# Kernel tuning notes

Measured on AMD Instinct MI355X. Metric: run time of the kernel, lower is better.

Reference implementation:

```python
import jax, jax.numpy as jnp
import numpy as np

N, G, E, D, H = 50000, 1000, 400000, 128, 256


def _sample_negatives(edge_index, batch, rng):
    # Vectorized equivalent of the torch per-edge loop: for each positive edge,
    # draw a dst in the same graph as src, excluding src itself and src's
    # existing neighbors, via 8 rounds of rejection sampling.
    src = edge_index[0]
    counts = np.bincount(batch, minlength=G)
    starts = np.concatenate([[0], np.cumsum(counts)[:-1]])
    g = batch[src]
    edge_keys = np.unique(edge_index[0].astype(np.int64) * N + edge_index[1])
    dst = src.copy()
    valid = np.zeros(E, dtype=bool)
    for _ in range(8):
        cand = starts[g] + rng.integers(0, counts[g])
        ok = (cand != src) & ~np.isin(src.astype(np.int64) * N + cand, edge_keys)
        take = ok & ~valid
        dst = np.where(take, cand, dst)
        valid |= ok
    fallback = starts[g] + (src - starts[g] + 1) % counts[g]  # deterministic in-graph node != src (when graph>1)
    dst = np.where(valid, dst, fallback)
    return np.stack([src, dst]).astype(np.int64)


def setup_inputs() -> dict:
    rng = np.random.default_rng(0)
    batch = np.sort(rng.integers(0, G, size=N)).astype(np.int64)  # contiguous graph ids
    counts = np.bincount(batch, minlength=G)
    starts = np.concatenate([[0], np.cumsum(counts)[:-1]])
    src = rng.integers(0, N, size=E)
    gsrc = batch[src]
    dst = starts[gsrc] + rng.integers(0, counts[gsrc])  # same-graph positive edges
    edge_index = np.stack([src, dst]).astype(np.int64)
    neg_edge_index = _sample_negatives(edge_index, batch, rng)

    key = jax.random.key(0)
    ks = jax.random.split(key, 4)
    x = jax.random.normal(ks[0], (N, D), jnp.float32)
    w1 = jax.random.normal(ks[1], (2 * D, H), jnp.float32) / np.sqrt(2 * D)
    w2 = jax.random.normal(ks[2], (H, H // 2), jnp.float32) / np.sqrt(H)
    w3 = jax.random.normal(ks[3], (H // 2, 1), jnp.float32) / np.sqrt(H // 2)
    return {
        "x": x,
        "edge_index": jnp.asarray(edge_index),
        "batch": jnp.asarray(batch),
        "neg_edge_index": jnp.asarray(neg_edge_index),
        "w1": w1, "b1": jnp.zeros((H,), jnp.float32),
        "g1": jnp.ones((H,), jnp.float32), "be1": jnp.zeros((H,), jnp.float32),
        "w2": w2, "b2": jnp.zeros((H // 2,), jnp.float32),
        "g2": jnp.ones((H // 2,), jnp.float32), "be2": jnp.zeros((H // 2,), jnp.float32),
        "w3": w3, "b3": jnp.zeros((1,), jnp.float32),
    }


def _layernorm(h, g, b, eps=1e-5):
    m = jnp.mean(h, axis=-1, keepdims=True)
    v = jnp.mean(jnp.square(h - m), axis=-1, keepdims=True)
    return (h - m) * jax.lax.rsqrt(v + eps) * g + b


def _edge_mlp(feat, w1, b1, g1, be1, w2, b2, g2, be2, w3, b3):
    h = jax.nn.relu(_layernorm(feat @ w1 + b1, g1, be1))
    h = jax.nn.relu(_layernorm(h @ w2 + b2, g2, be2))
    return jax.nn.sigmoid(h @ w3 + b3)


def reference(x, edge_index, batch, neg_edge_index, w1, b1, g1, be1, w2, b2, g2, be2, w3, b3):
    # batch is consumed by the (setup-time) negative sampler; kept for signature fidelity.
    all_idx = jnp.concatenate([edge_index, neg_edge_index], axis=1)  # [2, 2E]
    feat = jnp.concatenate([x[all_idx[0]], x[all_idx[1]]], axis=-1)  # [2E, 2D]
    pred = _edge_mlp(feat, w1, b1, g1, be1, w2, b2, g2, be2, w3, b3)  # [2E, 1]
    num_pos = edge_index.shape[1]
    num_neg = neg_edge_index.shape[1]
    labels = jnp.concatenate(
        [jnp.ones((num_pos, 1), pred.dtype), jnp.zeros((num_neg, 1), pred.dtype)], axis=0
    )
    return pred, labels
```

## Files before the change

### kernel.cpp

```cpp
#include <hip/hip_runtime.h>
#include <math.h>
#include <stdint.h>

#define NN    50000
#define EPOS  400000
#define ROWS  800000
#define DIM   128
#define D2    256
#define H1C   256
#define H2C   128
#define MT    64
#define NTH   512

typedef __bf16 bf16;
typedef __bf16 bf16x8 __attribute__((ext_vector_type(8)));
typedef __bf16 bf16x4 __attribute__((ext_vector_type(4)));
typedef float  f32x4  __attribute__((ext_vector_type(4)));

#define XB_N   (NN*DIM)
#define W1F_E  XB_N
#define W1F_N  (H1C*D2)
#define W2F_E  (XB_N + W1F_N)
#define W2F_N  (H2C*H1C)
#define WS_NEEDED ((size_t)(XB_N + W1F_N + W2F_N) * 2)

#define AOFF  0
#define SCR   32768
#define SCR2  34816
#define CFOFF 35840
#define SMEM_BYTES 40960

__device__ __forceinline__ void gll16(const void* g, void* l) {
    __builtin_amdgcn_global_load_lds(
        (const __attribute__((address_space(1))) void*)g,
        (__attribute__((address_space(3))) void*)l, 16, 0, 0);
}

__global__ void preconv(const float* __restrict__ x, const float* __restrict__ w1,
                        const float* __restrict__ w2, bf16* __restrict__ ws) {
    int i = blockIdx.x * 256 + threadIdx.x;
    if (i < XB_N) { ws[i] = (bf16)x[i]; return; }
    i -= XB_N;
    if (i < W1F_N) {
        int j = i & 7, l = (i >> 3) & 63, ct = i >> 9;
        int c = ct >> 4, t = ct & 15;
        int n = t * 16 + (l & 15);
        int k = c * 32 + (l >> 4) * 8 + j;
        ws[W1F_E + i] = (bf16)w1[k * H1C + n];
        return;
    }
    i -= W1F_N;
    if (i < W2F_N) {
        int j = i & 7, l = (i >> 3) & 63, ct = i >> 9;
        int c = ct >> 3, t = ct & 7;
        int n = t * 16 + (l & 15);
        int k = c * 32 + (l >> 4) * 8 + j;
        ws[W2F_E + i] = (bf16)w2[k * H2C + n];
    }
}

__global__ __launch_bounds__(NTH, 4) void lp_mfma8(
    const bf16* __restrict__ xb, const bf16* __restrict__ w1f, const bf16* __restrict__ w2f,
    const int*  __restrict__ ei, const int* __restrict__ nei,
    const float* __restrict__ b1, const float* __restrict__ g1, const float* __restrict__ be1,
    const float* __restrict__ b2, const float* __restrict__ g2, const float* __restrict__ be2,
    const float* __restrict__ w3, const float* __restrict__ b3,
    float* __restrict__ out)
{
    extern __shared__ char smem[];
    const int tid  = threadIdx.x;
    const int lane = tid & 63;
    const int w    = tid >> 6;
    const int wm   = w >> 2;
    const int wn   = w & 3;
    const int gr0  = blockIdx.x * MT;
    const int l15  = lane & 15;
    const int l4   = lane >> 4;

    #pragma unroll
    for (int ii = 0; ii < 4; ++ii) {
        const int i = w * 4 + ii;
        uint32_t doff = (uint32_t)(i << 10) + (uint32_t)(lane << 4);
        uint32_t loff = doff ^ (((doff >> 9) & 7u) << 4);
        int row = loff >> 9;
        int inb = loff & 511;
        int gr  = gr0 + row;
        int node;
        if (inb < 256) { node = (gr < EPOS) ? ei[gr]        : nei[gr - EPOS]; }
        else           { node = (gr < EPOS) ? ei[EPOS + gr] : nei[gr]; inb -= 256; }
        gll16((const char*)xb + (((size_t)node) << 8) + inb, smem + AOFF + (i << 10));
    }

    for (int i = tid; i < 1280; i += NTH) {
        float v;
        if      (i < 256)  v = b1[i];
        else if (i < 512)  v = g1[i - 256];
        else if (i < 768)  v = be1[i - 512];
        else if (i < 896)  v = b2[i - 768];
        else if (i < 1024) v = g2[i - 896];
        else if (i < 1152) v = be2[i - 1024];
        else               v = w3[i - 1152];
        *(float*)(smem + CFOFF + i * 4) = v;
    }

    uint32_t abase[2], asw[2];
    #pragma unroll
    for (int mi = 0; mi < 2; ++mi) {
        int row = (wm << 5) + (mi << 4) + l15;
        abase[mi] = (uint32_t)row << 9;
        asw[mi]   = (uint32_t)(row & 7) << 4;
    }
    const uint32_t koff  = (uint32_t)l4 << 4;
    const uint32_t c1off = ((uint32_t)wn << 8) + ((uint32_t)l4 << 4);
    const uint32_t c2off = ((uint32_t)wn << 7) + ((uint32_t)l4 << 4);

    __syncthreads();

    f32x4 acc1s[2][4] = {};
    const bf16* bp1 = w1f + (wn << 11) + (lane << 3);
    #pragma unroll
    for (int c = 0; c < 8; ++c) {
        bf16x8 af[2];
        #pragma unroll
        for (int mi = 0; mi < 2; ++mi)
            af[mi] = *(const bf16x8*)(smem + AOFF + ((abase[mi] + ((uint32_t)c << 6) + koff) ^ asw[mi]));
        #pragma unroll
        for (int ni = 0; ni < 4; ++ni) {
            bf16x8 bfr = *(const bf16x8*)(bp1 + (c << 13) + (ni << 9));
            #pragma unroll
            for (int mi = 0; mi < 2; ++mi)
                acc1s[mi][ni] = __builtin_amdgcn_mfma_f32_16x16x32_bf16(
                    bfr, af[mi], acc1s[mi][ni], 0, 0, 0);
        }
    }

    #pragma unroll
    for (int mi = 0; mi < 2; ++mi) {
        float s1 = 0.f, s2 = 0.f;
        #pragma unroll
        for (int ni = 0; ni < 4; ++ni) {
            f32x4 bias = *(const f32x4*)(smem + CFOFF + c1off + (ni << 6));
            #pragma unroll
            for (int j = 0; j < 4; ++j) {
                float v = acc1s[mi][ni][j] + bias[j];
                acc1s[mi][ni][j] = v;
                s1 += v; s2 += v * v;
            }
        }
        s1 += __shfl_xor(s1, 16); s1 += __shfl_xor(s1, 32);
        s2 += __shfl_xor(s2, 16); s2 += __shfl_xor(s2, 32);
        if (l4 == 0) {
            int row = (wm << 5) + (mi << 4) + l15;
            *(float2*)(smem + SCR + (row << 5) + (wn << 3)) = make_float2(s1, s2);
        }
    }
    __syncthreads();

    #pragma unroll
    for (int mi = 0; mi < 2; ++mi) {
        int row = (wm << 5) + (mi << 4) + l15;
        f32x4 p0 = *(const f32x4*)(smem + SCR + (row << 5));
        f32x4 p1 = *(const f32x4*)(smem + SCR + (row << 5) + 16);
        float s1 = p0[0] + p0[2] + p1[0] + p1[2];
        float s2 = p0[1] + p0[3] + p1[1] + p1[3];
        float mean = s1 * (1.f / 256.f);
        float var  = s2 * (1.f / 256.f) - mean * mean;
        float rstd = rsqrtf(var + 1e-5f);
        #pragma unroll
        for (int ni = 0; ni < 4; ++ni) {
            f32x4 gv  = *(const f32x4*)(smem + CFOFF + 1024 + c1off + (ni << 6));
            f32x4 bev = *(const f32x4*)(smem + CFOFF + 2048 + c1off + (ni << 6));
            bf16x4 hb;
            #pragma unroll
            for (int j = 0; j < 4; ++j) {
                float h = (acc1s[mi][ni][j] - mean) * rstd * gv[j] + bev[j];
                hb[j] = (bf16)fmaxf(h, 0.f);
            }
            uint32_t byte = ((uint32_t)row << 9) + ((uint32_t)wn << 7) + ((uint32_t)ni << 5) + ((uint32_t)l4 << 3);
            byte ^= ((byte >> 9) & 7u) << 4;
            *(bf16x4*)(smem + AOFF + byte) = hb;
        }
    }
    __syncthreads();

    f32x4 acc2s[2][2] = {};
    const bf16* bp2 = w2f + (wn << 10) + (lane << 3);
    #pragma unroll
    for (int c = 0; c < 8; ++c) {
        bf16x8 a2[2];
        #pragma unroll
        for (int mi = 0; mi < 2; ++mi)
            a2[mi] = *(const bf16x8*)(smem + AOFF + ((abase[mi] + ((uint32_t)c << 6) + koff) ^ asw[mi]));
        #pragma unroll
        for (int ni = 0; ni < 2; ++ni) {
            bf16x8 b2r = *(const bf16x8*)(bp2 + (c << 12) + (ni << 9));
            #pragma unroll
            for (int mi = 0; mi < 2; ++mi)
                acc2s[mi][ni] = __builtin_amdgcn_mfma_f32_16x16x32_bf16(
                    b2r, a2[mi], acc2s[mi][ni], 0, 0, 0);
        }
    }

    #pragma unroll
    for (int mi = 0; mi < 2; ++mi) {
        float s1 = 0.f, s2 = 0.f;
        #pragma unroll
        for (int ni = 0; ni < 2; ++ni) {
            f32x4 bias = *(const f32x4*)(smem + CFOFF + 3072 + c2off + (ni << 6));
            #pragma unroll
            for (int j = 0; j < 4; ++j) {
                float v = acc2s[mi][ni][j] + bias[j];
                acc2s[mi][ni][j] = v;
                s1 += v; s2 += v * v;
            }
        }
        s1 += __shfl_xor(s1, 16); s1 += __shfl_xor(s1, 32);
        s2 += __shfl_xor(s2, 16); s2 += __shfl_xor(s2, 32);
        if (l4 == 0) {
            int row = (wm << 5) + (mi << 4) + l15;
            *(float2*)(smem + SCR + (row << 5) + (wn << 3)) = make_float2(s1, s2);
        }
    }
    __syncthreads();

    #pragma unroll
    for (int mi = 0; mi < 2; ++mi) {
        int row = (wm << 5) + (mi << 4) + l15;
        f32x4 p0 = *(const f32x4*)(smem + SCR + (row << 5));
        f32x4 p1 = *(const f32x4*)(smem + SCR + (row << 5) + 16);
        float s1 = p0[0] + p0[2] + p1[0] + p1[2];
        float s2 = p0[1] + p0[3] + p1[1] + p1[3];
        float mean = s1 * (1.f / 128.f);
        float var  = s2 * (1.f / 128.f) - mean * mean;
        float rstd = rsqrtf(var + 1e-5f);
        float zp = 0.f;
        #pragma unroll
        for (int ni = 0; ni < 2; ++ni) {
            f32x4 gv  = *(const f32x4*)(smem + CFOFF + 3584 + c2off + (ni << 6));
            f32x4 bev = *(const f32x4*)(smem + CFOFF + 4096 + c2off + (ni << 6));
            f32x4 wv  = *(const f32x4*)(smem + CFOFF + 4608 + c2off + (ni << 6));
            #pragma unroll
            for (int j = 0; j < 4; ++j) {
                float h = (acc2s[mi][ni][j] - mean) * rstd * gv[j] + bev[j];
                h = fmaxf(h, 0.f);
                zp += h * wv[j];
            }
        }
        zp += __shfl_xor(zp, 16); zp += __shfl_xor(zp, 32);
        if (l4 == 0)
            *(float*)(smem + SCR2 + (row << 4) + (wn << 2)) = zp;
    }
    __syncthreads();

    if (wn == 0) {
        const float b3s = b3[0];
        #pragma unroll
        for (int mi = 0; mi < 2; ++mi) {
            int row = (wm << 5) + (mi << 4) + l15;
            int gr  = gr0 + row;
            if (l4 == 0) {
                f32x4 zv = *(const f32x4*)(smem + SCR2 + (row << 4));
                float z = zv[0] + zv[1] + zv[2] + zv[3] + b3s;
                out[gr] = 1.f / (1.f + expf(-z));
            } else if (l4 == 1) {
                out[ROWS + gr] = (gr < EPOS) ? 1.f : 0.f;
            }
        }
    }
}

#define TILE  32
#define PAD   264
__global__ __launch_bounds__(256, 4) void lp_fused(
    const float* __restrict__ x, const int* __restrict__ ei, const int* __restrict__ nei,
    const float* __restrict__ w1, const float* __restrict__ b1,
    const float* __restrict__ g1, const float* __restrict__ be1,
    const float* __restrict__ w2, const float* __restrict__ b2,
    const float* __restrict__ g2, const float* __restrict__ be2,
    const float* __restrict__ w3, const float* __restrict__ b3,
    float* __restrict__ out)
{
    __shared__ float lds[TILE][PAD];
    const int t = threadIdx.x, e = t >> 3, jg = t & 7;
    const int row = blockIdx.x * TILE + e;
    {
        int src, dst;
        if (row < EPOS) { src = ei[row];         dst = ei[EPOS + row]; }
        else            { src = nei[row - EPOS]; dst = nei[row]; }
        const float* base = (jg < 4) ? (x + src * DIM + jg * 32) : (x + dst * DIM + (jg - 4) * 32);
        const float4* b4 = (const float4*)base;
        #pragma unroll
        for (int s = 0; s < 8; ++s) *(float4*)&lds[e][jg * 32 + s * 4] = b4[s];
    }
    __syncthreads();
    float acc[32];
    #pragma unroll
    for (int i = 0; i < 32; ++i) acc[i] = 0.f;
    const int j0 = jg * 32;
    for (int k4 = 0; k4 < D2 / 4; ++k4) {
        float4 a4 = *(const float4*)&lds[e][k4 * 4];
        float av[4] = {a4.x, a4.y, a4.z, a4.w};
        #pragma unroll
        for (int kk = 0; kk < 4; ++kk) {
            const float a = av[kk];
            const float4* wr = (const float4*)(w1 + (k4 * 4 + kk) * H1C + j0);
            #pragma unroll
            for (int ii = 0; ii < 8; ++ii) {
                float4 wv = wr[ii];
                acc[ii*4+0] += a*wv.x; acc[ii*4+1] += a*wv.y; acc[ii*4+2] += a*wv.z; acc[ii*4+3] += a*wv.w;
            }
        }
    }
    float s1 = 0.f, s2 = 0.f;
    #pragma unroll
    for (int i = 0; i < 32; ++i) { float h = acc[i] + b1[j0+i]; acc[i] = h; s1 += h; s2 += h*h; }
    #pragma unroll
    for (int m = 1; m < 8; m <<= 1) { s1 += __shfl_xor(s1, m, 8); s2 += __shfl_xor(s2, m, 8); }
    float mean = s1 * (1.f/256.f), var = s2 * (1.f/256.f) - mean*mean, rstd = rsqrtf(var + 1e-5f);
    __syncthreads();
    #pragma unroll
    for (int i = 0; i < 32; ++i)
        lds[e][j0+i] = fmaxf((acc[i]-mean)*rstd*g1[j0+i]+be1[j0+i], 0.f);
    __syncthreads();
    float acc2[16];
    #pragma unroll
    for (int i = 0; i < 16; ++i) acc2[i] = 0.f;
    const int q0 = jg * 16;
    for (int k4 = 0; k4 < H1C / 4; ++k4) {
        float4 a4 = *(const float4*)&lds[e][k4 * 4];
        float av[4] = {a4.x, a4.y, a4.z, a4.w};
        #pragma unroll
        for (int kk = 0; kk < 4; ++kk) {
            const float a = av[kk];
            const float4* wr = (const float4*)(w2 + (k4 * 4 + kk) * H2C + q0);
            #pragma unroll
            for (int ii = 0; ii < 4; ++ii) {
                float4 wv = wr[ii];
                acc2[ii*4+0] += a*wv.x; acc2[ii*4+1] += a*wv.y; acc2[ii*4+2] += a*wv.z; acc2[ii*4+3] += a*wv.w;
            }
        }
    }
    s1 = 0.f; s2 = 0.f;
    #pragma unroll
    for (int i = 0; i < 16; ++i) { float h = acc2[i] + b2[q0+i]; acc2[i] = h; s1 += h; s2 += h*h; }
    #pragma unroll
    for (int m = 1; m < 8; m <<= 1) { s1 += __shfl_xor(s1, m, 8); s2 += __shfl_xor(s2, m, 8); }
    mean = s1 * (1.f/128.f); var = s2 * (1.f/128.f) - mean*mean; rstd = rsqrtf(var + 1e-5f);
    float zp = 0.f;
    #pragma unroll
    for (int i = 0; i < 16; ++i) {
        float h = fmaxf((acc2[i]-mean)*rstd*g2[q0+i]+be2[q0+i], 0.f);
        zp += h * w3[q0+i];
    }
    #pragma unroll
    for (int m = 1; m < 8; m <<= 1) zp += __shfl_xor(zp, m, 8);
    if (jg == 0) out[row] = 1.f / (1.f + expf(-(zp + b3[0])));
    if (jg == 1) out[ROWS + row] = (row < EPOS) ? 1.f : 0.f;
}

extern "C" void kernel_launch(void* const* d_in, const int* in_sizes, int n_in,
                              void* d_out, int out_size, void* d_ws, size_t ws_size,
                              hipStream_t stream) {
    const float* x   = (const float*)d_in[0];
    const int*   ei  = (const int*)d_in[1];
    const int*   nei = (const int*)d_in[3];
    const float* w1  = (const float*)d_in[4];
    const float* b1  = (const float*)d_in[5];
    const float* g1  = (const float*)d_in[6];
    const float* be1 = (const float*)d_in[7];
    const float* w2  = (const float*)d_in[8];
    const float* b2  = (const float*)d_in[9];
    const float* g2  = (const float*)d_in[10];
    const float* be2 = (const float*)d_in[11];
    const float* w3  = (const float*)d_in[12];
    const float* b3  = (const float*)d_in[13];
    float* out = (float*)d_out;

    if (ws_size >= WS_NEEDED) {
        bf16* ws = (bf16*)d_ws;
        const int total = XB_N + W1F_N + W2F_N;
        hipLaunchKernelGGL(preconv, dim3((total + 255) / 256), dim3(256), 0, stream,
                           x, w1, w2, ws);
        hipFuncSetAttribute((const void*)lp_mfma8,
                            hipFuncAttributeMaxDynamicSharedMemorySize, SMEM_BYTES);
        hipLaunchKernelGGL(lp_mfma8, dim3(ROWS / MT), dim3(NTH), SMEM_BYTES, stream,
                           ws, ws + W1F_E, ws + W2F_E, ei, nei,
                           b1, g1, be1, b2, g2, be2, w3, b3, out);
    } else {
        hipLaunchKernelGGL(lp_fused, dim3(ROWS / TILE), dim3(256), 0, stream,
                           x, ei, nei, w1, b1, g1, be1, w2, b2, g2, be2, w3, b3, out);
    }
}
```

Before: 264.9 us.

## Make MLP kernel persistent with double-buffered gather prefetch of next tile

Launches a fixed grid of 512 blocks, each looping over row tiles in a grid-stride loop. It uses two LDS buffers so the global_load_lds gather of the next tile's node features overlaps compute on the current tile. Bias is now folded into the MFMA accumulator initialisation instead of being added after the matmul. LDS per block roughly doubles, which lowers resident blocks per CU, and 25-vs-24 tiles per block adds some tail imbalance.

After: 872.6 us. 229% more time.

```diff
diff --git a/kernel.cpp b/kernel.cpp
--- a/kernel.cpp
+++ b/kernel.cpp
@@ -11,6 +11,8 @@
 #define H2C   128
 #define MT    64
 #define NTH   512
+#define TILES (ROWS/MT)
+#define GRID  512
 
 typedef __bf16 bf16;
 typedef __bf16 bf16x8 __attribute__((ext_vector_type(8)));
@@ -24,11 +26,10 @@
 #define W2F_N  (H2C*H1C)
 #define WS_NEEDED ((size_t)(XB_N + W1F_N + W2F_N) * 2)
 
-#define AOFF  0
-#define SCR   32768
-#define SCR2  34816
-#define CFOFF 35840
-#define SMEM_BYTES 40960
+#define SCR   65536
+#define SCR2  67584
+#define CFOFF 68608
+#define SMEM_BYTES 73728
 
 __device__ __forceinline__ void gll16(const void* g, void* l) {
     __builtin_amdgcn_global_load_lds(
@@ -59,7 +60,7 @@
     }
 }
 
-__global__ __launch_bounds__(NTH, 4) void lp_mfma8(
+__global__ __launch_bounds__(NTH, 4) void lp_mfma10(
     const bf16* __restrict__ xb, const bf16* __restrict__ w1f, const bf16* __restrict__ w2f,
     const int*  __restrict__ ei, const int* __restrict__ nei,
     const float* __restrict__ b1, const float* __restrict__ g1, const float* __restrict__ be1,
@@ -73,23 +74,24 @@
     const int w    = tid >> 6;
     const int wm   = w >> 2;
     const int wn   = w & 3;
-    const int gr0  = blockIdx.x * MT;
     const int l15  = lane & 15;
     const int l4   = lane >> 4;
 
-    #pragma unroll
-    for (int ii = 0; ii < 4; ++ii) {
-        const int i = w * 4 + ii;
-        uint32_t doff = (uint32_t)(i << 10) + (uint32_t)(lane << 4);
-        uint32_t loff = doff ^ (((doff >> 9) & 7u) << 4);
-        int row = loff >> 9;
-        int inb = loff & 511;
-        int gr  = gr0 + row;
-        int node;
-        if (inb < 256) { node = (gr < EPOS) ? ei[gr]        : nei[gr - EPOS]; }
-        else           { node = (gr < EPOS) ? ei[EPOS + gr] : nei[gr]; inb -= 256; }
-        gll16((const char*)xb + (((size_t)node) << 8) + inb, smem + AOFF + (i << 10));
-    }
+    auto stage = [&](int tile, uint32_t base) {
+        #pragma unroll
+        for (int ii = 0; ii < 4; ++ii) {
+            const int i = w * 4 + ii;
+            uint32_t doff = (uint32_t)(i << 10) + (uint32_t)(lane << 4);
+            uint32_t loff = doff ^ (((doff >> 9) & 7u) << 4);
+            int row = loff >> 9;
+            int inb = loff & 511;
+            int gr  = tile * MT + row;
+            int node;
+            if (inb < 256) { node = (gr < EPOS) ? ei[gr]        : nei[gr - EPOS]; }
+            else           { node = (gr < EPOS) ? ei[EPOS + gr] : nei[gr]; inb -= 256; }
+            gll16((const char*)xb + (((size_t)node) << 8) + inb, smem + base + (i << 10));
+        }
+    };
 
     for (int i = tid; i < 1280; i += NTH) {
         float v;
@@ -102,6 +104,7 @@
         else               v = w3[i - 1152];
         *(float*)(smem + CFOFF + i * 4) = v;
     }
+    stage(blockIdx.x, 0);
 
     uint32_t abase[2], asw[2];
     #pragma unroll
@@ -113,159 +116,171 @@
     const uint32_t koff  = (uint32_t)l4 << 4;
     const uint32_t c1off = ((uint32_t)wn << 8) + ((uint32_t)l4 << 4);
     const uint32_t c2off = ((uint32_t)wn << 7) + ((uint32_t)l4 << 4);
+    const float b3s = b3[0];
 
     __syncthreads();
 
-    f32x4 acc1s[2][4] = {};
-    const bf16* bp1 = w1f + (wn << 11) + (lane << 3);
-    #pragma unroll
-    for (int c = 0; c < 8; ++c) {
-        bf16x8 af[2];
-        #pragma unroll
-        for (int mi = 0; mi < 2; ++mi)
-            af[mi] = *(const bf16x8*)(smem + AOFF + ((abase[mi] + ((uint32_t)c << 6) + koff) ^ asw[mi]));
-        #pragma unroll
-        for (int ni = 0; ni < 4; ++ni) {
-            bf16x8 bfr = *(const bf16x8*)(bp1 + (c << 13) + (ni << 9));
-            #pragma unroll
-            for (int mi = 0; mi < 2; ++mi)
-                acc1s[mi][ni] = __builtin_amdgcn_mfma_f32_16x16x32_bf16(
-                    bfr, af[mi], acc1s[mi][ni], 0, 0, 0);
-        }
-    }
-
-    #pragma unroll
-    for (int mi = 0; mi < 2; ++mi) {
-        float s1 = 0.f, s2 = 0.f;
+    int cur = 0;
+    for (int t = blockIdx.x; t < TILES; t += GRID) {
+        const uint32_t abuf = (uint32_t)cur << 15;
+        const int nt = t + GRID;
+        if (nt < TILES) stage(nt, abuf ^ 32768u);
+
+        f32x4 acc1s[2][4];
         #pragma unroll
         for (int ni = 0; ni < 4; ++ni) {
             f32x4 bias = *(const f32x4*)(smem + CFOFF + c1off + (ni << 6));
-            #pragma unroll
-            for (int j = 0; j < 4; ++j) {
-                float v = acc1s[mi][ni][j] + bias[j];
-                acc1s[mi][ni][j] = v;
-                s1 += v; s2 += v * v;
-            }
-        }
-        s1 += __shfl_xor(s1, 16); s1 += __shfl_xor(s1, 32);
-        s2 += __shfl_xor(s2, 16); s2 += __shfl_xor(s2, 32);
-        if (l4 == 0) {
+            acc1s[0][ni] = bias; acc1s[1][ni] = bias;
+        }
+        const bf16* bp1 = w1f + (wn << 11) + (lane << 3);
+        #pragma unroll
+        for (int c = 0; c < 8; ++c) {
+            bf16x8 af[2];
+            #pragma unroll
+            for (int mi = 0; mi < 2; ++mi)
+                af[mi] = *(const bf16x8*)(smem + abuf + ((abase[mi] + ((uint32_t)c << 6) + koff) ^ asw[mi]));
+            #pragma unroll
+            for (int ni = 0; ni < 4; ++ni) {
+                bf16x8 bfr = *(const bf16x8*)(bp1 + (c << 13) + (ni << 9));
+                #pragma unroll
+                for (int mi = 0; mi < 2; ++mi)
+                    acc1s[mi][ni] = __builtin_amdgcn_mfma_f32_16x16x32_bf16(
+                        bfr, af[mi], acc1s[mi][ni], 0, 0, 0);
+            }
+        }
+
+        #pragma unroll
+        for (int mi = 0; mi < 2; ++mi) {
+            float s1 = 0.f, s2 = 0.f;
+            #pragma unroll
+            for (int ni = 0; ni < 4; ++ni)
+                #pragma unroll
+                for (int j = 0; j < 4; ++j) {
+                    float v = acc1s[mi][ni][j];
+                    s1 += v; s2 += v * v;
+                }
+            s1 += __shfl_xor(s1, 16); s1 += __shfl_xor(s1, 32);
+            s2 += __shfl_xor(s2, 16); s2 += __shfl_xor(s2, 32);
+            if (l4 == 0) {
+                int row = (wm << 5) + (mi << 4) + l15;
+                *(float2*)(smem + SCR + (row << 5) + (wn << 3)) = make_float2(s1, s2);
+            }
+        }
+        __syncthreads();
+
+        #pragma unroll
+        for (int mi = 0; mi < 2; ++mi) {
             int row = (wm << 5) + (mi << 4) + l15;
-            *(float2*)(smem + SCR + (row << 5) + (wn << 3)) = make_float2(s1, s2);
-        }
-    }
-    __syncthreads();
-
-    #pragma unroll
-    for (int mi = 0; mi < 2; ++mi) {
-        int row = (wm << 5) + (mi << 4) + l15;
-        f32x4 p0 = *(const f32x4*)(smem + SCR + (row << 5));
-        f32x4 p1 = *(const f32x4*)(smem + SCR + (row << 5) + 16);
-        float s1 = p0[0] + p0[2] + p1[0] + p1[2];
-        float s2 = p0[1] + p0[3] + p1[1] + p1[3];
-        float mean = s1 * (1.f / 256.f);
-        float var  = s2 * (1.f / 256.f) - mean * mean;
-        float rstd = rsqrtf(var + 1e-5f);
-        #pragma unroll
-        for (int ni = 0; ni < 4; ++ni) {
-            f32x4 gv  = *(const f32x4*)(smem + CFOFF + 1024 + c1off + (ni << 6));
-            f32x4 bev = *(const f32x4*)(smem + CFOFF + 2048 + c1off + (ni << 6));
-            bf16x4 hb;
-            #pragma unroll
-            for (int j = 0; j < 4; ++j) {
-                float h = (acc1s[mi][ni][j] - mean) * rstd * gv[j] + bev[j];
-                hb[j] = (bf16)fmaxf(h, 0.f);
-            }
-            uint32_t byte = ((uint32_t)row << 9) + ((uint32_t)wn << 7) + ((uint32_t)ni << 5) + ((uint32_t)l4 << 3);
-            byte ^= ((byte >> 9) & 7u) << 4;
-            *(bf16x4*)(smem + AOFF + byte) = hb;
-        }
-    }
-    __syncthreads();
-
-    f32x4 acc2s[2][2] = {};
-    const bf16* bp2 = w2f + (wn << 10) + (lane << 3);
-    #pragma unroll
-    for (int c = 0; c < 8; ++c) {
-        bf16x8 a2[2];
-        #pragma unroll
-        for (int mi = 0; mi < 2; ++mi)
-            a2[mi] = *(const bf16x8*)(smem + AOFF + ((abase[mi] + ((uint32_t)c << 6) + koff) ^ asw[mi]));
-        #pragma unroll
-        for (int ni = 0; ni < 2; ++ni) {
-            bf16x8 b2r = *(const bf16x8*)(bp2 + (c << 12) + (ni << 9));
-            #pragma unroll
-            for (int mi = 0; mi < 2; ++mi)
-                acc2s[mi][ni] = __builtin_amdgcn_mfma_f32_16x16x32_bf16(
-                    b2r, a2[mi], acc2s[mi][ni], 0, 0, 0);
-        }
-    }
-
-    #pragma unroll
-    for (int mi = 0; mi < 2; ++mi) {
-        float s1 = 0.f, s2 = 0.f;
+            f32x4 p0 = *(const f32x4*)(smem + SCR + (row << 5));
+            f32x4 p1 = *(const f32x4*)(smem + SCR + (row << 5) + 16);
+            float s1 = p0[0] + p0[2] + p1[0] + p1[2];
+            float s2 = p0[1] + p0[3] + p1[1] + p1[3];
+            float mean = s1 * (1.f / 256.f);
+            float var  = s2 * (1.f / 256.f) - mean * mean;
+            float rstd = rsqrtf(var + 1e-5f);
+            #pragma unroll
+            for (int ni = 0; ni < 4; ++ni) {
+                f32x4 gv  = *(const f32x4*)(smem + CFOFF + 1024 + c1off + (ni << 6));
+                f32x4 bev = *(const f32x4*)(smem + CFOFF + 2048 + c1off + (ni << 6));
+                bf16x4 hb;
+                #pragma unroll
+                for (int j = 0; j < 4; ++j) {
+                    float h = (acc1s[mi][ni][j] - mean) * rstd * gv[j] + bev[j];
+                    hb[j] = (bf16)fmaxf(h, 0.f);
+                }
+                uint32_t byte = ((uint32_t)row << 9) + ((uint32_t)wn << 7) + ((uint32_t)ni << 5) + ((uint32_t)l4 << 3);
+                byte ^= ((byte >> 9) & 7u) << 4;
+                *(bf16x4*)(smem + abuf + byte) = hb;
+            }
+        }
+        __syncthreads();
+
+        f32x4 acc2s[2][2];
         #pragma unroll
         for (int ni = 0; ni < 2; ++ni) {
             f32x4 bias = *(const f32x4*)(smem + CFOFF + 3072 + c2off + (ni << 6));
-            #pragma unroll
-            for (int j = 0; j < 4; ++j) {
-                float v = acc2s[mi][ni][j] + bias[j];
-                acc2s[mi][ni][j] = v;
-                s1 += v; s2 += v * v;
-            }
-        }
-        s1 += __shfl_xor(s1, 16); s1 += __shfl_xor(s1, 32);
-        s2 += __shfl_xor(s2, 16); s2 += __shfl_xor(s2, 32);
-        if (l4 == 0) {
-            int row = (wm << 5) + (mi << 4) + l15;
-            *(float2*)(smem + SCR + (row << 5) + (wn << 3)) = make_float2(s1, s2);
-        }
-    }
-    __syncthreads();
-
-    #pragma unroll
-    for (int mi = 0; mi < 2; ++mi) {
-        int row = (wm << 5) + (mi << 4) + l15;
-        f32x4 p0 = *(const f32x4*)(smem + SCR + (row << 5));
-        f32x4 p1 = *(const f32x4*)(smem + SCR + (row << 5) + 16);
-        float s1 = p0[0] + p0[2] + p1[0] + p1[2];
-        float s2 = p0[1] + p0[3] + p1[1] + p1[3];
-        float mean = s1 * (1.f / 128.f);
-        float var  = s2 * (1.f / 128.f) - mean * mean;
-        float rstd = rsqrtf(var + 1e-5f);
-        float zp = 0.f;
-        #pragma unroll
-        for (int ni = 0; ni < 2; ++ni) {
-            f32x4 gv  = *(const f32x4*)(smem + CFOFF + 3584 + c2off + (ni << 6));
-            f32x4 bev = *(const f32x4*)(smem + CFOFF + 4096 + c2off + (ni << 6));
-            f32x4 wv  = *(const f32x4*)(smem + CFOFF + 4608 + c2off + (ni << 6));
-            #pragma unroll
-            for (int j = 0; j < 4; ++j) {
-                float h = (acc2s[mi][ni][j] - mean) * rstd * gv[j] + bev[j];
-                h = fmaxf(h, 0.f);
-                zp += h * wv[j];
-            }
-        }
-        zp += __shfl_xor(zp, 16); zp += __shfl_xor(zp, 32);
-        if (l4 == 0)
-            *(float*)(smem + SCR2 + (row << 4) + (wn << 2)) = zp;
-    }
-    __syncthreads();
-
-    if (wn == 0) {
-        const float b3s = b3[0];
+            acc2s[0][ni] = bias; acc2s[1][ni] = bias;
+        }
+        const bf16* bp2 = w2f + (wn << 10) + (lane << 3);
+        #pragma unroll
+        for (int c = 0; c < 8; ++c) {
+            bf16x8 a2[2];
+            #pragma unroll
+            for (int mi = 0; mi < 2; ++mi)
+                a2[mi] = *(const bf16x8*)(smem + abuf + ((abase[mi] + ((uint32_t)c << 6) + koff) ^ asw[mi]));
+            #pragma unroll
+            for (int ni = 0; ni < 2; ++ni) {
+                bf16x8 b2r = *(const bf16x8*)(bp2 + (c << 12) + (ni << 9));
+                #pragma unroll
+                for (int mi = 0; mi < 2; ++mi)
+                    acc2s[mi][ni] = __builtin_amdgcn_mfma_f32_16x16x32_bf16(
+                        b2r, a2[mi], acc2s[mi][ni], 0, 0, 0);
+            }
+        }
+
+        #pragma unroll
+        for (int mi = 0; mi < 2; ++mi) {
+            float s1 = 0.f, s2 = 0.f;
+            #pragma unroll
+            for (int ni = 0; ni < 2; ++ni)
+                #pragma unroll
+                for (int j = 0; j < 4; ++j) {
+                    float v = acc2s[mi][ni][j];
+                    s1 += v; s2 += v * v;
+                }
+            s1 += __shfl_xor(s1, 16); s1 += __shfl_xor(s1, 32);
+            s2 += __shfl_xor(s2, 16); s2 += __shfl_xor(s2, 32);
+            if (l4 == 0) {
+                int row = (wm << 5) + (mi << 4) + l15;
+                *(float2*)(smem + SCR + (row << 5) + (wn << 3)) = make_float2(s1, s2);
+            }
+        }
+        __syncthreads();
+
         #pragma unroll
         for (int mi = 0; mi < 2; ++mi) {
             int row = (wm << 5) + (mi << 4) + l15;
-            int gr  = gr0 + row;
-            if (l4 == 0) {
-                f32x4 zv = *(const f32x4*)(smem + SCR2 + (row << 4));
-                float z = zv[0] + zv[1] + zv[2] + zv[3] + b3s;
-                out[gr] = 1.f / (1.f + expf(-z));
-            } else if (l4 == 1) {
-                out[ROWS + gr] = (gr < EPOS) ? 1.f : 0.f;
-            }
-        }
+            f32x4 p0 = *(const f32x4*)(smem + SCR + (row << 5));
+            f32x4 p1 = *(const f32x4*)(smem + SCR + (row << 5) + 16);
+            float s1 = p0[0] + p0[2] + p1[0] + p1[2];
+            float s2 = p0[1] + p0[3] + p1[1] + p1[3];
+            float mean = s1 * (1.f / 128.f);
+            float var  = s2 * (1.f / 128.f) - mean * mean;
+            float rstd = rsqrtf(var + 1e-5f);
+            float zp = 0.f;
+            #pragma unroll
+            for (int ni = 0; ni < 2; ++ni) {
+                f32x4 gv  = *(const f32x4*)(smem + CFOFF + 3584 + c2off + (ni << 6));
+                f32x4 bev = *(const f32x4*)(smem + CFOFF + 4096 + c2off + (ni << 6));
+                f32x4 wv  = *(const f32x4*)(smem + CFOFF + 4608 + c2off + (ni << 6));
+                #pragma unroll
+                for (int j = 0; j < 4; ++j) {
+                    float h = (acc2s[mi][ni][j] - mean) * rstd * gv[j] + bev[j];
+                    h = fmaxf(h, 0.f);
+                    zp += h * wv[j];
+                }
+            }
+            zp += __shfl_xor(zp, 16); zp += __shfl_xor(zp, 32);
+            if (l4 == 0)
+                *(float*)(smem + SCR2 + (row << 4) + (wn << 2)) = zp;
+        }
+        __syncthreads();
+
+        if (wn == 0) {
+            #pragma unroll
+            for (int mi = 0; mi < 2; ++mi) {
+                int row = (wm << 5) + (mi << 4) + l15;
+                int gr  = t * MT + row;
+                if (l4 == 0) {
+                    f32x4 zv = *(const f32x4*)(smem + SCR2 + (row << 4));
+                    float z = zv[0] + zv[1] + zv[2] + zv[3] + b3s;
+                    out[gr] = 1.f / (1.f + expf(-z));
+                } else if (l4 == 1) {
+                    out[ROWS + gr] = (gr < EPOS) ? 1.f : 0.f;
+                }
+            }
+        }
+        cur ^= 1;
     }
 }
 
@@ -381,9 +396,9 @@
         const int total = XB_N + W1F_N + W2F_N;
         hipLaunchKernelGGL(preconv, dim3((total + 255) / 256), dim3(256), 0, stream,
                            x, w1, w2, ws);
-        hipFuncSetAttribute((const void*)lp_mfma8,
+        hipFuncSetAttribute((const void*)lp_mfma10,
                             hipFuncAttributeMaxDynamicSharedMemorySize, SMEM_BYTES);
-        hipLaunchKernelGGL(lp_mfma8, dim3(ROWS / MT), dim3(NTH), SMEM_BYTES, stream,
+        hipLaunchKernelGGL(lp_mfma10, dim3(GRID), dim3(NTH), SMEM_BYTES, stream,
                            ws, ws + W1F_E, ws + W2F_E, ei, nei,
                            b1, g1, be1, b2, g2, be2, w3, b3, out);
     } else {
```
